# Kernel optimization log

Hardware: AMD Instinct MI355X
Metric: run time of the kernel (lower is better)

The kernel has to match this reference:

```python
import jax, jax.numpy as jnp
import numpy as np

B, SQ, SK, D_MODEL, H, D = 2, 2048, 2048, 1024, 16, 64


def setup_inputs() -> dict:
    key = jax.random.key(0)
    ks = jax.random.split(key, 10)
    s = 1.0 / np.sqrt(D_MODEL)
    return {
        "x": jax.random.normal(ks[0], (B, SK, D_MODEL), jnp.float32),
        "x2": jax.random.normal(ks[1], (B, SQ, D_MODEL), jnp.float32),
        "Wq": jax.random.normal(ks[2], (H, D_MODEL, D), jnp.float32) * s,
        "bq": jax.random.normal(ks[3], (H, D), jnp.float32) * s,
        "Wk": jax.random.normal(ks[4], (H, D_MODEL, D), jnp.float32) * s,
        "bk": jax.random.normal(ks[5], (H, D), jnp.float32) * s,
        "Wv": jax.random.normal(ks[6], (H, D_MODEL, D), jnp.float32) * s,
        "bv": jax.random.normal(ks[7], (H, D), jnp.float32) * s,
        "Wo": jax.random.normal(ks[8], (D_MODEL, D_MODEL), jnp.float32) * s,
        "bo": jax.random.normal(ks[9], (D_MODEL,), jnp.float32) * s,
    }


def reference(x, x2, Wq, bq, Wk, bk, Wv, bv, Wo, bo):
    # Batched per-head projections (fuses the Python per-head loop).
    # q: [B, H, SQ, D]; k,v: [B, H, SK, D]
    q = jnp.einsum("bsm,hmd->bhsd", x2, Wq) + bq[None, :, None, :]
    k = jnp.einsum("bsm,hmd->bhsd", x, Wk) + bk[None, :, None, :]
    v = jnp.einsum("bsm,hmd->bhsd", x, Wv) + bv[None, :, None, :]
    scale = 1.0 / jnp.sqrt(jnp.asarray(D, q.dtype))
    scores = jnp.einsum("bhqd,bhkd->bhqk", q, k) * scale  # [B,H,SQ,SK]
    attn = jax.nn.softmax(scores, axis=-1)
    o = jnp.einsum("bhqk,bhkd->bhqd", attn, v)  # [B,H,SQ,D]
    # concat heads along feature dim (head-major order matches torch.cat)
    o = o.transpose(0, 2, 1, 3).reshape(B, SQ, H * D)
    # final projection; dropout is identity in eval mode
    return o @ Wo.T + bo
```

## Files before the change

kernel.cpp:

```cpp
#include <hip/hip_runtime.h>
#include <math.h>

#define B_   2
#define SQ_  2048
#define SK_  2048
#define DM_  1024
#define H_   16
#define D_   64

typedef __attribute__((ext_vector_type(8))) short bf16x8;
typedef __attribute__((ext_vector_type(4))) float f32x4;
typedef unsigned int u32;

__device__ __forceinline__ short f2bf(float f) {
    union { float f; unsigned u; } v; v.f = f;
    unsigned r = v.u + 0x7FFFu + ((v.u >> 16) & 1u);
    return (short)(r >> 16);
}
__device__ __forceinline__ u32 pk2bf(float x, float y) {
    union { float f; u32 u; } a, b; a.f = x; b.f = y;
    return ((a.u + 0x8000u) >> 16) | ((b.u + 0x8000u) & 0xFFFF0000u);
}

__device__ __forceinline__ void gll16(const void* g, void* l) {
    __builtin_amdgcn_global_load_lds(
        (const __attribute__((address_space(1))) u32*)g,
        (__attribute__((address_space(3))) u32*)l, 16, 0, 0);
}

__global__ __launch_bounds__(256) void prep_kernel(
    const float* __restrict__ Wq, const float* __restrict__ Wk,
    const float* __restrict__ Wv, const float* __restrict__ Wo,
    const float* __restrict__ x,  const float* __restrict__ x2,
    short* __restrict__ WqT, short* __restrict__ WkT,
    short* __restrict__ WvT, short* __restrict__ Wob,
    short* __restrict__ xb,  short* __restrict__ x2b)
{
    const int t = threadIdx.x;
    const int z = blockIdx.z;
    if (z >= 3) {
        const float* src = (z == 3) ? Wo : (z == 4) ? x : x2;
        short* dst       = (z == 3) ? Wob : (z == 4) ? xb : x2b;
        int nloop = (z == 3) ? 4 : 16;
        int bid = blockIdx.y * 16 + blockIdx.x;
        #pragma unroll 4
        for (int j = 0; j < nloop; j++) {
            int i = bid * (nloop * 256) + j * 256 + t;
            float4 v = ((const float4*)src)[i];
            short4 s;
            s.x = f2bf(v.x); s.y = f2bf(v.y); s.z = f2bf(v.z); s.w = f2bf(v.w);
            ((short4*)dst)[i] = s;
        }
        return;
    }
    const float* W = (z == 0) ? Wq : (z == 1) ? Wk : Wv;
    short* WT      = (z == 0) ? WqT : (z == 1) ? WkT : WvT;
    const int h  = blockIdx.y;
    const int m0 = blockIdx.x * 64;
    __shared__ short Ls[64][68];

    #pragma unroll
    for (int it = 0; it < 4; it++) {
        int lin = it * 256 + t;
        int m = lin >> 4, d4 = lin & 15;
        float4 v = *(const float4*)&W[((long)h * DM_ + m0 + m) * D_ + d4 * 4];
        short4 s;
        s.x = f2bf(v.x); s.y = f2bf(v.y); s.z = f2bf(v.z); s.w = f2bf(v.w);
        *(short4*)&Ls[m][d4 * 4] = s;
    }
    __syncthreads();
    #pragma unroll
    for (int it = 0; it < 2; it++) {
        int d = (t >> 3) + it * 32, scol = t & 7;
        bf16x8 vv;
        #pragma unroll
        for (int j = 0; j < 8; j++) vv[j] = Ls[scol * 8 + j][d];
        *(bf16x8*)&WT[((long)h * 64 + d) * DM_ + m0 + scol * 8] = vv;
    }
}

__global__ __launch_bounds__(256) void vtrans_kernel(
    const short* __restrict__ Vb, short* __restrict__ VT)
{
    const int bh = blockIdx.y;
    const int b  = bh >> 4, h = bh & 15;
    const int s0 = blockIdx.x * 64;
    const int t  = threadIdx.x;
    __shared__ short Ls[64][68];

    #pragma unroll
    for (int it = 0; it < 2; it++) {
        int lin = it * 256 + t;
        int s = lin >> 3, c8 = lin & 7;
        bf16x8 v = *(const bf16x8*)&Vb[((long)(b * 2048 + s0 + s)) * 1024 + h * 64 + c8 * 8];
        short4 a, c;
        a.x = v[0]; a.y = v[1]; a.z = v[2]; a.w = v[3];
        c.x = v[4]; c.y = v[5]; c.z = v[6]; c.w = v[7];
        *(short4*)&Ls[s][c8 * 8]     = a;
        *(short4*)&Ls[s][c8 * 8 + 4] = c;
    }
    __syncthreads();
    #pragma unroll
    for (int it = 0; it < 2; it++) {
        int d = (t >> 3) + it * 32, scol = t & 7;
        bf16x8 vv;
        #pragma unroll
        for (int j = 0; j < 8; j++) vv[j] = Ls[scol * 8 + j][d];
        *(bf16x8*)&VT[((long)bh * 64 + d) * 2048 + s0 + scol * 8] = vv;
    }
}

template <bool BF16_OUT>
__device__ __forceinline__ void gemm_core(
    const short* __restrict__ A, const short* __restrict__ Bw,
    const float* __restrict__ bias, void* __restrict__ outp,
    int r0, int n0, float oscale)
{
    __shared__ short As[128 * 64];
    __shared__ short Bs[128 * 64];

    const int t    = threadIdx.x;
    const int w    = t >> 6;
    const int ln   = t & 63;
    const int l15  = ln & 15;
    const int quad = ln >> 4;
    const int wr   = w >> 1;
    const int wc   = w & 1;

    f32x4 acc[4][4];
    #pragma unroll
    for (int i = 0; i < 4; i++)
        #pragma unroll
        for (int j = 0; j < 4; j++) acc[i][j] = (f32x4){0.f, 0.f, 0.f, 0.f};

    const int srow = ln >> 3;
    const int sc   = (ln & 7) ^ srow;
    const int rsw  = l15 & 7;

    for (int k0 = 0; k0 < 1024; k0 += 64) {
        __syncthreads();
        #pragma unroll
        for (int j = 0; j < 4; j++) {
            int q   = w * 4 + j;
            int row = q * 8 + srow;
            gll16(A  + ((long)(r0 + row) << 10) + k0 + sc * 8, As + q * 512);
            gll16(Bw + ((long)(n0 + row) << 10) + k0 + sc * 8, Bs + q * 512);
        }
        __syncthreads();
        #pragma unroll
        for (int kh = 0; kh < 2; kh++) {
            bf16x8 af[4], bfr[4];
            #pragma unroll
            for (int i = 0; i < 4; i++) {
                int ra = wr * 64 + i * 16 + l15;
                int rb = wc * 64 + i * 16 + l15;
                int pc = ((kh * 4 + quad) ^ rsw) * 8;
                af[i]  = *(const bf16x8*)&As[ra * 64 + pc];
                bfr[i] = *(const bf16x8*)&Bs[rb * 64 + pc];
            }
            #pragma unroll
            for (int i = 0; i < 4; i++)
                #pragma unroll
                for (int j = 0; j < 4; j++)
                    acc[i][j] = __builtin_amdgcn_mfma_f32_16x16x32_bf16(
                        af[i], bfr[j], acc[i][j], 0, 0, 0);
        }
    }

    #pragma unroll
    for (int j = 0; j < 4; j++) {
        int col = n0 + wc * 64 + j * 16 + l15;
        float bv = bias[col];
        #pragma unroll
        for (int i = 0; i < 4; i++) {
            int rowb = r0 + wr * 64 + i * 16 + quad * 4;
            #pragma unroll
            for (int r = 0; r < 4; r++) {
                float v = (acc[i][j][r] + bv) * oscale;
                if (BF16_OUT)
                    ((short*)outp)[(long)(rowb + r) * 1024 + col] = f2bf(v);
                else
                    ((float*)outp)[(long)(rowb + r) * 1024 + col] = v;
            }
        }
    }
}

#define QSCALE 0.180336880977f

__global__ __launch_bounds__(256) void gemm_qkv_kernel(
    const short* __restrict__ x2b, const short* __restrict__ xb,
    const short* __restrict__ WqT, const short* __restrict__ WkT,
    const short* __restrict__ WvT,
    const float* __restrict__ bq, const float* __restrict__ bk,
    const float* __restrict__ bv,
    short* __restrict__ Qb, short* __restrict__ Kb, short* __restrict__ Vb)
{
    const int z = blockIdx.z;
    const short* A    = (z == 0) ? x2b : xb;
    const short* Bw   = (z == 0) ? WqT : (z == 1) ? WkT : WvT;
    const float* bias = (z == 0) ? bq  : (z == 1) ? bk  : bv;
    short* outp       = (z == 0) ? Qb  : (z == 1) ? Kb  : Vb;
    const float scl   = (z == 0) ? QSCALE : 1.0f;
    gemm_core<true>(A, Bw, bias, outp, blockIdx.x * 128, blockIdx.y * 128, scl);
}

__global__ __launch_bounds__(256) void gemm_out_kernel(
    const short* __restrict__ A, const short* __restrict__ Wob,
    const float* __restrict__ bo, float* __restrict__ out)
{
    gemm_core<false>(A, Wob, bo, out, blockIdx.x * 128, blockIdx.y * 128, 1.0f);
}

__global__ __launch_bounds__(256) void flash_kernel(
    const short* __restrict__ Q, const short* __restrict__ K,
    const short* __restrict__ VT, short* __restrict__ O)
{
    const int t    = threadIdx.x;
    const int wave = t >> 6;
    const int ln   = t & 63;
    const int l15  = ln & 15;
    const int quad = ln >> 4;
    const int bh = blockIdx.y;
    const int b  = bh >> 4;
    const int h  = bh & 15;
    const int q0 = blockIdx.x * 64;
    const int wq = q0 + wave * 16;

    __shared__ short Ks[64 * 64];
    __shared__ short Vs[64 * 64];
    __shared__ short Ps[4][16 * 72];

    const int srow = ln >> 3;
    const int sc   = (ln & 7) ^ srow;
    const int rsw  = l15 & 7;

    bf16x8 aQ0, aQ1;
    {
        const short* Qp = Q + ((long)(b * SQ_ + wq + l15)) * 1024 + h * 64 + quad * 8;
        aQ0 = *(const bf16x8*)(Qp);
        aQ1 = *(const bf16x8*)(Qp + 32);
    }

    bf16x8 ones;
    #pragma unroll
    for (int j = 0; j < 8; j++) ones[j] = (short)0x3F80;

    f32x4 o_acc[4];
    #pragma unroll
    for (int i = 0; i < 4; i++) o_acc[i] = (f32x4){0.f, 0.f, 0.f, 0.f};
    f32x4 l_acc = (f32x4){0.f, 0.f, 0.f, 0.f};

    const short* Kbase = K  + ((long)b * SK_) * 1024 + h * 64;
    const short* Vbase = VT + (long)bh * D_ * SK_;

    for (int k0 = 0; k0 < SK_; k0 += 64) {
        __syncthreads();
        #pragma unroll
        for (int it = 0; it < 2; ++it) {
            int qq  = wave * 2 + it;
            int row = qq * 8 + srow;
            gll16(Kbase + (long)(k0 + row) * 1024 + sc * 8, Ks + qq * 512);
            gll16(Vbase + (long)row * 2048 + k0 + sc * 8,   Vs + qq * 512);
        }
        __syncthreads();

        f32x4 st[4];
        #pragma unroll
        for (int kt = 0; kt < 4; kt++) {
            const short* kr = &Ks[(kt * 16 + l15) * 64];
            bf16x8 ka0 = *(const bf16x8*)&kr[((quad    ) ^ rsw) * 8];
            bf16x8 ka1 = *(const bf16x8*)&kr[((quad + 4) ^ rsw) * 8];
            f32x4 z = (f32x4){0.f, 0.f, 0.f, 0.f};
            z = __builtin_amdgcn_mfma_f32_16x16x32_bf16(ka0, aQ0, z, 0, 0, 0);
            z = __builtin_amdgcn_mfma_f32_16x16x32_bf16(ka1, aQ1, z, 0, 0, 0);
            st[kt] = z;
        }

        short* pr = &Ps[wave][l15 * 72];
        #pragma unroll
        for (int kt = 0; kt < 4; kt++) {
            float p0 = __builtin_amdgcn_exp2f(st[kt][0]);
            float p1 = __builtin_amdgcn_exp2f(st[kt][1]);
            float p2 = __builtin_amdgcn_exp2f(st[kt][2]);
            float p3 = __builtin_amdgcn_exp2f(st[kt][3]);
            uint2 wv; wv.x = pk2bf(p0, p1); wv.y = pk2bf(p2, p3);
            *(uint2*)&pr[(4 * kt + quad) * 4] = wv;
        }

        bf16x8 aP0 = *(const bf16x8*)&pr[quad * 8];
        bf16x8 aP1 = *(const bf16x8*)&pr[(quad + 4) * 8];
        l_acc = __builtin_amdgcn_mfma_f32_16x16x32_bf16(aP0, ones, l_acc, 0, 0, 0);
        l_acc = __builtin_amdgcn_mfma_f32_16x16x32_bf16(aP1, ones, l_acc, 0, 0, 0);
        #pragma unroll
        for (int dt = 0; dt < 4; dt++) {
            const short* vr = &Vs[(dt * 16 + l15) * 64];
            bf16x8 bv0 = *(const bf16x8*)&vr[((quad    ) ^ rsw) * 8];
            bf16x8 bv1 = *(const bf16x8*)&vr[((quad + 4) ^ rsw) * 8];
            o_acc[dt] = __builtin_amdgcn_mfma_f32_16x16x32_bf16(aP0, bv0, o_acc[dt], 0, 0, 0);
            o_acc[dt] = __builtin_amdgcn_mfma_f32_16x16x32_bf16(aP1, bv1, o_acc[dt], 0, 0, 0);
        }
    }

    #pragma unroll
    for (int r = 0; r < 4; r++) {
        float inv = 1.0f / l_acc[r];
        long row = (long)b * SQ_ + wq + quad * 4 + r;
        short* Op = O + row * 1024 + h * 64 + l15;
        #pragma unroll
        for (int dt = 0; dt < 4; dt++)
            Op[dt * 16] = f2bf(o_acc[dt][r] * inv);
    }
}

extern "C" void kernel_launch(void* const* d_in, const int* in_sizes, int n_in,
                              void* d_out, int out_size, void* d_ws, size_t ws_size,
                              hipStream_t stream) {
    const float* x  = (const float*)d_in[0];
    const float* x2 = (const float*)d_in[1];
    const float* Wq = (const float*)d_in[2];
    const float* bq = (const float*)d_in[3];
    const float* Wk = (const float*)d_in[4];
    const float* bk = (const float*)d_in[5];
    const float* Wv = (const float*)d_in[6];
    const float* bv = (const float*)d_in[7];
    const float* Wo = (const float*)d_in[8];
    const float* bo = (const float*)d_in[9];
    float* out = (float*)d_out;

    const size_t nAct = (size_t)B_ * SK_ * DM_;
    const size_t nW   = (size_t)DM_ * DM_;
    short* bufA = (short*)d_ws;
    short* bufB = bufA + nAct;
    short* Qb   = bufB + nAct;
    short* Kb   = Qb + nAct;
    short* Vb   = Kb + nAct;
    short* WqT  = Vb + nAct;
    short* WkT  = WqT + nW;
    short* WvT  = WkT + nW;
    short* Wob  = WvT + nW;

    prep_kernel<<<dim3(16, 16, 6), 256, 0, stream>>>(
        Wq, Wk, Wv, Wo, x, x2, WqT, WkT, WvT, Wob, bufA, bufB);

    gemm_qkv_kernel<<<dim3(32, 8, 3), 256, 0, stream>>>(
        bufB, bufA, WqT, WkT, WvT, bq, bk, bv, Qb, Kb, Vb);

    vtrans_kernel<<<dim3(32, 32), 256, 0, stream>>>(Vb, bufA);
    flash_kernel<<<dim3(32, 32), 256, 0, stream>>>(Qb, Kb, bufA, bufB);
    gemm_out_kernel<<<dim3(32, 8), 256, 0, stream>>>(bufB, Wob, bo, out);
}
```

Measured before the change: 231.1 us.

## Fuse V transpose into QKV GEMM epilogue and retile output GEMM

The V projection epilogue now writes directly in transposed [b,h,d,s] layout with short4 stores, removing the separate vtrans kernel launch and its extra read and write of V. The output projection gets its own kernel using 64x128 tiles, doubling the grid to 512 blocks for better CU occupancy on the 1024-wide output. The transposed epilogue stores are strided along the sequence dimension, so they may coalesce less well. The smaller output tile also reuses less data per block.

```diff
diff --git a/kernel.cpp b/kernel.cpp
--- a/kernel.cpp
+++ b/kernel.cpp
@@ -79,38 +79,7 @@
     }
 }
 
-__global__ __launch_bounds__(256) void vtrans_kernel(
-    const short* __restrict__ Vb, short* __restrict__ VT)
-{
-    const int bh = blockIdx.y;
-    const int b  = bh >> 4, h = bh & 15;
-    const int s0 = blockIdx.x * 64;
-    const int t  = threadIdx.x;
-    __shared__ short Ls[64][68];
-
-    #pragma unroll
-    for (int it = 0; it < 2; it++) {
-        int lin = it * 256 + t;
-        int s = lin >> 3, c8 = lin & 7;
-        bf16x8 v = *(const bf16x8*)&Vb[((long)(b * 2048 + s0 + s)) * 1024 + h * 64 + c8 * 8];
-        short4 a, c;
-        a.x = v[0]; a.y = v[1]; a.z = v[2]; a.w = v[3];
-        c.x = v[4]; c.y = v[5]; c.z = v[6]; c.w = v[7];
-        *(short4*)&Ls[s][c8 * 8]     = a;
-        *(short4*)&Ls[s][c8 * 8 + 4] = c;
-    }
-    __syncthreads();
-    #pragma unroll
-    for (int it = 0; it < 2; it++) {
-        int d = (t >> 3) + it * 32, scol = t & 7;
-        bf16x8 vv;
-        #pragma unroll
-        for (int j = 0; j < 8; j++) vv[j] = Ls[scol * 8 + j][d];
-        *(bf16x8*)&VT[((long)bh * 64 + d) * 2048 + s0 + scol * 8] = vv;
-    }
-}
-
-template <bool BF16_OUT>
+template <int MODE>
 __device__ __forceinline__ void gemm_core(
     const short* __restrict__ A, const short* __restrict__ Bw,
     const float* __restrict__ bias, void* __restrict__ outp,
@@ -171,16 +140,32 @@
     for (int j = 0; j < 4; j++) {
         int col = n0 + wc * 64 + j * 16 + l15;
         float bv = bias[col];
-        #pragma unroll
-        for (int i = 0; i < 4; i++) {
-            int rowb = r0 + wr * 64 + i * 16 + quad * 4;
-            #pragma unroll
-            for (int r = 0; r < 4; r++) {
-                float v = (acc[i][j][r] + bv) * oscale;
-                if (BF16_OUT)
-                    ((short*)outp)[(long)(rowb + r) * 1024 + col] = f2bf(v);
-                else
-                    ((float*)outp)[(long)(rowb + r) * 1024 + col] = v;
+        if (MODE == 2) {
+            int hh = col >> 6, dd = col & 63;
+            #pragma unroll
+            for (int i = 0; i < 4; i++) {
+                int rowb = r0 + wr * 64 + i * 16 + quad * 4;
+                int bb = rowb >> 11, ss = rowb & 2047;
+                short4 sv;
+                sv.x = f2bf(acc[i][j][0] + bv);
+                sv.y = f2bf(acc[i][j][1] + bv);
+                sv.z = f2bf(acc[i][j][2] + bv);
+                sv.w = f2bf(acc[i][j][3] + bv);
+                *(short4*)&((short*)outp)[
+                    ((long)(((bb << 4) + hh) * 64 + dd) << 11) + ss] = sv;
+            }
+        } else {
+            #pragma unroll
+            for (int i = 0; i < 4; i++) {
+                int rowb = r0 + wr * 64 + i * 16 + quad * 4;
+                #pragma unroll
+                for (int r = 0; r < 4; r++) {
+                    float v = (acc[i][j][r] + bv) * oscale;
+                    if (MODE == 0)
+                        ((short*)outp)[(long)(rowb + r) * 1024 + col] = f2bf(v);
+                    else
+                        ((float*)outp)[(long)(rowb + r) * 1024 + col] = v;
+                }
             }
         }
     }
@@ -194,22 +179,91 @@
     const short* __restrict__ WvT,
     const float* __restrict__ bq, const float* __restrict__ bk,
     const float* __restrict__ bv,
-    short* __restrict__ Qb, short* __restrict__ Kb, short* __restrict__ Vb)
+    short* __restrict__ Qb, short* __restrict__ Kb, short* __restrict__ VT)
 {
     const int z = blockIdx.z;
-    const short* A    = (z == 0) ? x2b : xb;
-    const short* Bw   = (z == 0) ? WqT : (z == 1) ? WkT : WvT;
-    const float* bias = (z == 0) ? bq  : (z == 1) ? bk  : bv;
-    short* outp       = (z == 0) ? Qb  : (z == 1) ? Kb  : Vb;
-    const float scl   = (z == 0) ? QSCALE : 1.0f;
-    gemm_core<true>(A, Bw, bias, outp, blockIdx.x * 128, blockIdx.y * 128, scl);
+    if (z == 0) {
+        gemm_core<0>(x2b, WqT, bq, Qb, blockIdx.x * 128, blockIdx.y * 128, QSCALE);
+    } else if (z == 1) {
+        gemm_core<0>(xb, WkT, bk, Kb, blockIdx.x * 128, blockIdx.y * 128, 1.0f);
+    } else {
+        gemm_core<2>(xb, WvT, bv, VT, blockIdx.x * 128, blockIdx.y * 128, 1.0f);
+    }
 }
 
 __global__ __launch_bounds__(256) void gemm_out_kernel(
-    const short* __restrict__ A, const short* __restrict__ Wob,
-    const float* __restrict__ bo, float* __restrict__ out)
+    const short* __restrict__ A, const short* __restrict__ Bw,
+    const float* __restrict__ bias, float* __restrict__ outp)
 {
-    gemm_core<false>(A, Wob, bo, out, blockIdx.x * 128, blockIdx.y * 128, 1.0f);
+    __shared__ short As[64 * 64];
+    __shared__ short Bs[128 * 64];
+
+    const int r0   = blockIdx.x * 64;
+    const int n0   = blockIdx.y * 128;
+    const int t    = threadIdx.x;
+    const int w    = t >> 6;
+    const int ln   = t & 63;
+    const int l15  = ln & 15;
+    const int quad = ln >> 4;
+    const int wr   = w >> 1;
+    const int wc   = w & 1;
+
+    f32x4 acc[2][4];
+    #pragma unroll
+    for (int i = 0; i < 2; i++)
+        #pragma unroll
+        for (int j = 0; j < 4; j++) acc[i][j] = (f32x4){0.f, 0.f, 0.f, 0.f};
+
+    const int srow = ln >> 3;
+    const int sc   = (ln & 7) ^ srow;
+    const int rsw  = l15 & 7;
+
+    for (int k0 = 0; k0 < 1024; k0 += 64) {
+        __syncthreads();
+        #pragma unroll
+        for (int j = 0; j < 6; j++) {
+            int q = w * 6 + j;
+            if (q < 8) {
+                int row = q * 8 + srow;
+                gll16(A + ((long)(r0 + row) << 10) + k0 + sc * 8, As + q * 512);
+            } else {
+                int qb = q - 8;
+                int row = qb * 8 + srow;
+                gll16(Bw + ((long)(n0 + row) << 10) + k0 + sc * 8, Bs + qb * 512);
+            }
+        }
+        __syncthreads();
+        #pragma unroll
+        for (int kh = 0; kh < 2; kh++) {
+            int pc = ((kh * 4 + quad) ^ rsw) * 8;
+            bf16x8 af[2], bfr[4];
+            #pragma unroll
+            for (int i = 0; i < 2; i++)
+                af[i] = *(const bf16x8*)&As[(wr * 32 + i * 16 + l15) * 64 + pc];
+            #pragma unroll
+            for (int j = 0; j < 4; j++)
+                bfr[j] = *(const bf16x8*)&Bs[(wc * 64 + j * 16 + l15) * 64 + pc];
+            #pragma unroll
+            for (int i = 0; i < 2; i++)
+                #pragma unroll
+                for (int j = 0; j < 4; j++)
+                    acc[i][j] = __builtin_amdgcn_mfma_f32_16x16x32_bf16(
+                        af[i], bfr[j], acc[i][j], 0, 0, 0);
+        }
+    }
+
+    #pragma unroll
+    for (int j = 0; j < 4; j++) {
+        int col = n0 + wc * 64 + j * 16 + l15;
+        float bv = bias[col];
+        #pragma unroll
+        for (int i = 0; i < 2; i++) {
+            int rowb = r0 + wr * 32 + i * 16 + quad * 4;
+            #pragma unroll
+            for (int r = 0; r < 4; r++)
+                outp[(long)(rowb + r) * 1024 + col] = acc[i][j][r] + bv;
+        }
+    }
 }
 
 __global__ __launch_bounds__(256) void flash_kernel(
@@ -334,8 +388,8 @@
     short* bufB = bufA + nAct;
     short* Qb   = bufB + nAct;
     short* Kb   = Qb + nAct;
-    short* Vb   = Kb + nAct;
-    short* WqT  = Vb + nAct;
+    short* VTws = Kb + nAct;
+    short* WqT  = VTws + nAct;
     short* WkT  = WqT + nW;
     short* WvT  = WkT + nW;
     short* Wob  = WvT + nW;
@@ -344,9 +398,8 @@
         Wq, Wk, Wv, Wo, x, x2, WqT, WkT, WvT, Wob, bufA, bufB);
 
     gemm_qkv_kernel<<<dim3(32, 8, 3), 256, 0, stream>>>(
-        bufB, bufA, WqT, WkT, WvT, bq, bk, bv, Qb, Kb, Vb);
-
-    vtrans_kernel<<<dim3(32, 32), 256, 0, stream>>>(Vb, bufA);
-    flash_kernel<<<dim3(32, 32), 256, 0, stream>>>(Qb, Kb, bufA, bufB);
-    gemm_out_kernel<<<dim3(32, 8), 256, 0, stream>>>(bufB, Wob, bo, out);
-}
+        bufB, bufA, WqT, WkT, WvT, bq, bk, bv, Qb, Kb, VTws);
+
+    flash_kernel<<<dim3(32, 32), 256, 0, stream>>>(Qb, Kb, VTws, bufB);
+    gemm_out_kernel<<<dim3(64, 8), 256, 0, stream>>>(bufB, Wob, bo, out);
+}
```

Result: faster. 223.8 us (-3.2%).
